# Performance work log

Measured on AMD Instinct MI355X. Metric: run time of the kernel, lower is better.

## Reference

```python
import jax, jax.numpy as jnp
import numpy as np

EPS = 1e-7


def setup_inputs() -> dict:
    key = jax.random.key(0)
    k1, k2, k3 = jax.random.split(key, 3)
    B, Nt, Nv, D = 64, 128, 256, 512
    text_feats = jax.random.normal(k1, (B, Nt, D), dtype=jnp.float32)
    visual_feats = jax.random.normal(k2, (B, Nv, D), dtype=jnp.float32)
    attention_mask = jax.random.randint(k3, (B, Nt), 0, 2, dtype=jnp.int32)
    return {"text_feats": text_feats, "visual_feats": visual_feats,
            "attention_mask": attention_mask}


def _l2norm(x):
    return x / jnp.clip(jnp.linalg.norm(x, axis=-1, keepdims=True), 1e-12)


def reference(text_feats, visual_feats, attention_mask):
    # Normalize token features (F.normalize along D)
    t = _l2norm(text_feats)            # (B, Nt, D)
    v = _l2norm(visual_feats)          # (B, Nv, D)
    # All-pairs token similarities: (B, B, Nt, Nv)
    token_sims = jnp.einsum('itd,jvd->ijtv', t, v)
    # Max over visual tokens -> (B, B, Nt)
    max_sims = jnp.max(token_sims, axis=3)
    # Masked mean over text tokens -> (B, B)
    mask = attention_mask.astype(jnp.float32)[:, None, :]   # (B, 1, Nt) broadcasts over pairs
    masked_sum = jnp.sum(max_sims * mask, axis=2)            # (B, B)
    valid = jnp.clip(jnp.sum(mask, axis=2), EPS)             # (B, 1)
    clip_sims = masked_sum / valid                           # (B, B)
    # Symmetric InfoNCE on the diagonal
    B = clip_sims.shape[0]
    diag = jnp.arange(B)
    losses_t2v = -jax.nn.log_softmax(clip_sims, axis=1)[diag, diag]
    losses_v2t = -jax.nn.log_softmax(clip_sims.T, axis=1)[diag, diag]
    contrastive_loss = jnp.mean(losses_t2v + losses_v2t) / 2.0
    # Regularization: keep negative token sims near zero
    neg_sims = jnp.clip(token_sims, -20.0, 0.0)
    reg_loss = 0.15 * jnp.mean(neg_sims ** 2)
    return contrastive_loss + reg_loss
```

## Files before the change

kernel.cpp:

```cpp
#include <hip/hip_runtime.h>
#include <hip/hip_bf16.h>

#define BB 64
#define NT 128
#define NV 256
#define DD 512
#define BK 32
#define EPSF 1e-7f

typedef __attribute__((ext_vector_type(8))) short bf16x8;
typedef __attribute__((ext_vector_type(4))) float f32x4;

__device__ __forceinline__ void glds16(const ushort* g, ushort* l) {
    __builtin_amdgcn_global_load_lds(
        (const __attribute__((address_space(1))) unsigned int*)g,
        (__attribute__((address_space(3))) unsigned int*)l, 16, 0, 0);
}

__global__ __launch_bounds__(256) void k_normalize(
    const float* __restrict__ tf, const float* __restrict__ vf,
    __hip_bfloat16* __restrict__ tn, __hip_bfloat16* __restrict__ vn) {
    int row = blockIdx.x;
    const float* src;
    __hip_bfloat16* dst;
    if (row < BB * NT) {
        src = tf + (size_t)row * DD;
        dst = tn + (size_t)row * DD;
    } else {
        int r = row - BB * NT;
        src = vf + (size_t)r * DD;
        dst = vn + (size_t)r * DD;
    }
    int tid = threadIdx.x;
    float2 x = ((const float2*)src)[tid];
    float ss = x.x * x.x + x.y * x.y;
    #pragma unroll
    for (int off = 32; off; off >>= 1) ss += __shfl_down(ss, off, 64);
    __shared__ float wsum[4];
    int lane = tid & 63, wid = tid >> 6;
    if (lane == 0) wsum[wid] = ss;
    __syncthreads();
    float tot = wsum[0] + wsum[1] + wsum[2] + wsum[3];
    float scale = 1.0f / fmaxf(sqrtf(tot), 1e-12f);
    __hip_bfloat162 o;
    o.x = __float2bfloat16(x.x * scale);
    o.y = __float2bfloat16(x.y * scale);
    ((__hip_bfloat162*)dst)[tid] = o;
}

__global__ __launch_bounds__(512, 2) void k_gemm(
    const __hip_bfloat16* __restrict__ tn, const __hip_bfloat16* __restrict__ vn,
    float* __restrict__ max_sims, float* __restrict__ reg_sum) {
    __shared__ ushort sT[NT][BK];
    __shared__ ushort sV[NV][BK];
    __shared__ float maxbuf[NT][4];
    __shared__ float redw[8];

    const int i = blockIdx.x, j = blockIdx.y;
    const int tid = threadIdx.x;
    const int l = tid & 63, w = tid >> 6;
    const int wr = w >> 2, wc = w & 3;
    const int m15 = l & 15, q = l >> 4;

    const ushort* tbase = (const ushort*)tn + (size_t)i * NT * DD;
    const ushort* vbase = (const ushort*)vn + (size_t)j * NV * DD;

    const int tf0 = tid * 8;
    const int tr = tf0 >> 5, tc = tf0 & 31;
    const int vf0a = tid * 8;
    const int vra = vf0a >> 5, vca = vf0a & 31;
    const int vf0b = (512 + tid) * 8;
    const int vrb = vf0b >> 5, vcb = vf0b & 31;

    f32x4 acc[4][4];
    #pragma unroll
    for (int rt = 0; rt < 4; ++rt)
        #pragma unroll
        for (int ct = 0; ct < 4; ++ct) acc[rt][ct] = (f32x4){0.f, 0.f, 0.f, 0.f};

    ushort* sTf = &sT[0][0];
    ushort* sVf = &sV[0][0];

    for (int kk = 0; kk < DD; kk += BK) {
        glds16(tbase + (size_t)tr * DD + kk + tc, sTf + tf0);
        glds16(vbase + (size_t)vra * DD + kk + vca, sVf + vf0a);
        glds16(vbase + (size_t)vrb * DD + kk + vcb, sVf + vf0b);
        __syncthreads();

        bf16x8 a[4], b[4];
        #pragma unroll
        for (int rt = 0; rt < 4; ++rt)
            a[rt] = *(const bf16x8*)&sT[wr * 64 + rt * 16 + m15][q * 8];
        #pragma unroll
        for (int ct = 0; ct < 4; ++ct)
            b[ct] = *(const bf16x8*)&sV[wc * 64 + ct * 16 + m15][q * 8];
        #pragma unroll
        for (int rt = 0; rt < 4; ++rt)
            #pragma unroll
            for (int ct = 0; ct < 4; ++ct)
                acc[rt][ct] = __builtin_amdgcn_mfma_f32_16x16x32_bf16(
                    a[rt], b[ct], acc[rt][ct], 0, 0, 0);
        __syncthreads();
    }

    float rp = 0.0f;
    #pragma unroll
    for (int rt = 0; rt < 4; ++rt)
        #pragma unroll
        for (int ct = 0; ct < 4; ++ct)
            #pragma unroll
            for (int r = 0; r < 4; ++r) {
                float m = fminf(acc[rt][ct][r], 0.0f);
                rp = fmaf(m, m, rp);
            }

    #pragma unroll
    for (int rt = 0; rt < 4; ++rt)
        #pragma unroll
        for (int r = 0; r < 4; ++r) {
            float m = acc[rt][0][r];
            #pragma unroll
            for (int ct = 1; ct < 4; ++ct) m = fmaxf(m, acc[rt][ct][r]);
            #pragma unroll
            for (int msk = 1; msk < 16; msk <<= 1)
                m = fmaxf(m, __shfl_xor(m, msk, 64));
            if (m15 == 0)
                maxbuf[wr * 64 + rt * 16 + q * 4 + r][wc] = m;
        }

    #pragma unroll
    for (int off = 32; off; off >>= 1) rp += __shfl_down(rp, off, 64);
    if (l == 0) redw[w] = rp;
    __syncthreads();

    if (tid < NT) {
        float m = fmaxf(fmaxf(maxbuf[tid][0], maxbuf[tid][1]),
                        fmaxf(maxbuf[tid][2], maxbuf[tid][3]));
        max_sims[((size_t)(i * BB + j)) * NT + tid] = m;
    }
    if (tid == 0) {
        float s = 0.0f;
        #pragma unroll
        for (int x = 0; x < 8; ++x) s += redw[x];
        atomicAdd(reg_sum, s);
    }
}

__global__ __launch_bounds__(NT) void k_clip(
    const float* __restrict__ max_sims, const int* __restrict__ mask,
    float* __restrict__ clip_sims) {
    int bx = blockIdx.x;
    int i = bx / BB;
    int t = threadIdx.x;
    float m = (float)mask[i * NT + t];
    float v = max_sims[(size_t)bx * NT + t] * m;
    #pragma unroll
    for (int off = 32; off; off >>= 1) {
        v += __shfl_down(v, off, 64);
        m += __shfl_down(m, off, 64);
    }
    __shared__ float a0[2], a1[2];
    int wid = t >> 6;
    if ((t & 63) == 0) { a0[wid] = v; a1[wid] = m; }
    __syncthreads();
    if (t == 0)
        clip_sims[bx] = (a0[0] + a0[1]) / fmaxf(a1[0] + a1[1], EPSF);
}

__global__ __launch_bounds__(256) void k_loss(
    const float* __restrict__ clip_sims, const float* __restrict__ reg_sum,
    float* __restrict__ out) {
    __shared__ float sc[BB][BB + 1];
    __shared__ float lrow[BB], lcol[BB];
    int tid = threadIdx.x;
    for (int idx = tid; idx < BB * BB; idx += 256)
        sc[idx / BB][idx % BB] = clip_sims[idx];
    __syncthreads();
    if (tid < BB) {
        int i = tid;
        float m = sc[i][0];
        #pragma unroll
        for (int j = 1; j < BB; ++j) m = fmaxf(m, sc[i][j]);
        float s = 0.0f;
        #pragma unroll
        for (int j = 0; j < BB; ++j) s += expf(sc[i][j] - m);
        lrow[i] = m + logf(s) - sc[i][i];
    } else if (tid < 2 * BB) {
        int i = tid - BB;
        float m = sc[0][i];
        #pragma unroll
        for (int j = 1; j < BB; ++j) m = fmaxf(m, sc[j][i]);
        float s = 0.0f;
        #pragma unroll
        for (int j = 0; j < BB; ++j) s += expf(sc[j][i] - m);
        lcol[i] = m + logf(s) - sc[i][i];
    }
    __syncthreads();
    if (tid == 0) {
        float tot = 0.0f;
        for (int i = 0; i < BB; ++i) tot += lrow[i] + lcol[i];
        float contrastive = tot / (2.0f * BB);
        double denom = (double)BB * BB * NT * NV;
        float reg = 0.15f * (float)((double)reg_sum[0] / denom);
        out[0] = contrastive + reg;
    }
}

extern "C" void kernel_launch(void* const* d_in, const int* in_sizes, int n_in,
                              void* d_out, int out_size, void* d_ws, size_t ws_size,
                              hipStream_t stream) {
    const float* tf = (const float*)d_in[0];
    const float* vf = (const float*)d_in[1];
    const int* mask = (const int*)d_in[2];
    float* out = (float*)d_out;

    char* ws = (char*)d_ws;
    size_t tn_bytes = (size_t)BB * NT * DD * sizeof(__hip_bfloat16);
    size_t vn_bytes = (size_t)BB * NV * DD * sizeof(__hip_bfloat16);
    size_t ms_bytes = (size_t)BB * BB * NT * sizeof(float);
    size_t cs_bytes = (size_t)BB * BB * sizeof(float);

    __hip_bfloat16* tn = (__hip_bfloat16*)ws;
    __hip_bfloat16* vn = (__hip_bfloat16*)(ws + tn_bytes);
    float* max_sims = (float*)(ws + tn_bytes + vn_bytes);
    float* clip_sims = (float*)(ws + tn_bytes + vn_bytes + ms_bytes);
    float* reg_sum = (float*)(ws + tn_bytes + vn_bytes + ms_bytes + cs_bytes);

    hipMemsetAsync(reg_sum, 0, sizeof(float), stream);

    k_normalize<<<BB * NT + BB * NV, 256, 0, stream>>>(tf, vf, tn, vn);
    k_gemm<<<dim3(BB, BB), 512, 0, stream>>>(tn, vn, max_sims, reg_sum);
    k_clip<<<BB * BB, NT, 0, stream>>>(max_sims, mask, clip_sims);
    k_loss<<<1, 256, 0, stream>>>(clip_sims, reg_sum, out);
}
```

Before: 272.9 us.

## Fuse masked mean into GEMM, use 256-thread blocks, and swizzle LDS tiles

After: 258.5 us. -5.3%, faster.

```diff
diff --git a/kernel.cpp b/kernel.cpp
--- a/kernel.cpp
+++ b/kernel.cpp
@@ -19,8 +19,10 @@
 
 __global__ __launch_bounds__(256) void k_normalize(
     const float* __restrict__ tf, const float* __restrict__ vf,
-    __hip_bfloat16* __restrict__ tn, __hip_bfloat16* __restrict__ vn) {
+    __hip_bfloat16* __restrict__ tn, __hip_bfloat16* __restrict__ vn,
+    float* __restrict__ reg_sum) {
     int row = blockIdx.x;
+    if (row == 0 && threadIdx.x == 0) *reg_sum = 0.0f;
     const float* src;
     __hip_bfloat16* dst;
     if (row < BB * NT) {
@@ -48,56 +50,85 @@
     ((__hip_bfloat162*)dst)[tid] = o;
 }
 
-__global__ __launch_bounds__(512, 2) void k_gemm(
+__global__ __launch_bounds__(256, 2) void k_gemm(
     const __hip_bfloat16* __restrict__ tn, const __hip_bfloat16* __restrict__ vn,
-    float* __restrict__ max_sims, float* __restrict__ reg_sum) {
+    const int* __restrict__ mask,
+    float* __restrict__ clip_sims, float* __restrict__ reg_sum) {
     __shared__ ushort sT[NT][BK];
     __shared__ ushort sV[NV][BK];
-    __shared__ float maxbuf[NT][4];
-    __shared__ float redw[8];
+    __shared__ float maxbuf[NT][2];
+    __shared__ float redw[4];
+    __shared__ float c0[2], c1[2];
 
     const int i = blockIdx.x, j = blockIdx.y;
     const int tid = threadIdx.x;
     const int l = tid & 63, w = tid >> 6;
-    const int wr = w >> 2, wc = w & 3;
+    const int wr = w >> 1, wc = w & 1;
     const int m15 = l & 15, q = l >> 4;
 
     const ushort* tbase = (const ushort*)tn + (size_t)i * NT * DD;
     const ushort* vbase = (const ushort*)vn + (size_t)j * NV * DD;
 
-    const int tf0 = tid * 8;
-    const int tr = tf0 >> 5, tc = tf0 & 31;
-    const int vf0a = tid * 8;
-    const int vra = vf0a >> 5, vca = vf0a & 31;
-    const int vf0b = (512 + tid) * 8;
-    const int vrb = vf0b >> 5, vcb = vf0b & 31;
-
-    f32x4 acc[4][4];
-    #pragma unroll
-    for (int rt = 0; rt < 4; ++rt)
-        #pragma unroll
-        for (int ct = 0; ct < 4; ++ct) acc[rt][ct] = (f32x4){0.f, 0.f, 0.f, 0.f};
-
     ushort* sTf = &sT[0][0];
     ushort* sVf = &sV[0][0];
 
+    int t_off[2], t_l[2];
+    #pragma unroll
+    for (int s = 0; s < 2; ++s) {
+        int f = s * 256 + tid;
+        int r = f >> 2, qp = f & 3;
+        int qs = qp ^ ((r >> 1) & 3);
+        t_off[s] = r * DD + qs * 8;
+        t_l[s] = f * 8;
+    }
+    int v_off[4], v_l[4];
+    #pragma unroll
+    for (int s = 0; s < 4; ++s) {
+        int f = s * 256 + tid;
+        int r = f >> 2, qp = f & 3;
+        int qs = qp ^ ((r >> 1) & 3);
+        v_off[s] = r * DD + qs * 8;
+        v_l[s] = f * 8;
+    }
+
+    int a_idx[4], b_idx[8];
+    #pragma unroll
+    for (int rt = 0; rt < 4; ++rt) {
+        int row = wr * 64 + rt * 16 + m15;
+        int qp = q ^ ((row >> 1) & 3);
+        a_idx[rt] = row * BK + qp * 8;
+    }
+    #pragma unroll
+    for (int ct = 0; ct < 8; ++ct) {
+        int row = wc * 128 + ct * 16 + m15;
+        int qp = q ^ ((row >> 1) & 3);
+        b_idx[ct] = row * BK + qp * 8;
+    }
+
+    f32x4 acc[4][8];
+    #pragma unroll
+    for (int rt = 0; rt < 4; ++rt)
+        #pragma unroll
+        for (int ct = 0; ct < 8; ++ct) acc[rt][ct] = (f32x4){0.f, 0.f, 0.f, 0.f};
+
     for (int kk = 0; kk < DD; kk += BK) {
-        glds16(tbase + (size_t)tr * DD + kk + tc, sTf + tf0);
-        glds16(vbase + (size_t)vra * DD + kk + vca, sVf + vf0a);
-        glds16(vbase + (size_t)vrb * DD + kk + vcb, sVf + vf0b);
+        #pragma unroll
+        for (int s = 0; s < 2; ++s)
+            glds16(tbase + t_off[s] + kk, sTf + t_l[s]);
+        #pragma unroll
+        for (int s = 0; s < 4; ++s)
+            glds16(vbase + v_off[s] + kk, sVf + v_l[s]);
         __syncthreads();
 
-        bf16x8 a[4], b[4];
+        bf16x8 a[4], b[8];
+        #pragma unroll
+        for (int rt = 0; rt < 4; ++rt) a[rt] = *(const bf16x8*)(sTf + a_idx[rt]);
+        #pragma unroll
+        for (int ct = 0; ct < 8; ++ct) b[ct] = *(const bf16x8*)(sVf + b_idx[ct]);
         #pragma unroll
         for (int rt = 0; rt < 4; ++rt)
-            a[rt] = *(const bf16x8*)&sT[wr * 64 + rt * 16 + m15][q * 8];
-        #pragma unroll
-        for (int ct = 0; ct < 4; ++ct)
-            b[ct] = *(const bf16x8*)&sV[wc * 64 + ct * 16 + m15][q * 8];
-        #pragma unroll
-        for (int rt = 0; rt < 4; ++rt)
-            #pragma unroll
-            for (int ct = 0; ct < 4; ++ct)
+            #pragma unroll
+            for (int ct = 0; ct < 8; ++ct)
                 acc[rt][ct] = __builtin_amdgcn_mfma_f32_16x16x32_bf16(
                     a[rt], b[ct], acc[rt][ct], 0, 0, 0);
         __syncthreads();
@@ -107,7 +138,7 @@
     #pragma unroll
     for (int rt = 0; rt < 4; ++rt)
         #pragma unroll
-        for (int ct = 0; ct < 4; ++ct)
+        for (int ct = 0; ct < 8; ++ct)
             #pragma unroll
             for (int r = 0; r < 4; ++r) {
                 float m = fminf(acc[rt][ct][r], 0.0f);
@@ -120,7 +151,7 @@
         for (int r = 0; r < 4; ++r) {
             float m = acc[rt][0][r];
             #pragma unroll
-            for (int ct = 1; ct < 4; ++ct) m = fmaxf(m, acc[rt][ct][r]);
+            for (int ct = 1; ct < 8; ++ct) m = fmaxf(m, acc[rt][ct][r]);
             #pragma unroll
             for (int msk = 1; msk < 16; msk <<= 1)
                 m = fmaxf(m, __shfl_xor(m, msk, 64));
@@ -134,37 +165,21 @@
     __syncthreads();
 
     if (tid < NT) {
-        float m = fmaxf(fmaxf(maxbuf[tid][0], maxbuf[tid][1]),
-                        fmaxf(maxbuf[tid][2], maxbuf[tid][3]));
-        max_sims[((size_t)(i * BB + j)) * NT + tid] = m;
-    }
+        float rm = fmaxf(maxbuf[tid][0], maxbuf[tid][1]);
+        float mf = (float)mask[i * NT + tid];
+        float v = rm * mf;
+        #pragma unroll
+        for (int off = 32; off; off >>= 1) {
+            v += __shfl_down(v, off, 64);
+            mf += __shfl_down(mf, off, 64);
+        }
+        if (l == 0) { c0[w] = v; c1[w] = mf; }
+    }
+    __syncthreads();
     if (tid == 0) {
-        float s = 0.0f;
-        #pragma unroll
-        for (int x = 0; x < 8; ++x) s += redw[x];
-        atomicAdd(reg_sum, s);
-    }
-}
-
-__global__ __launch_bounds__(NT) void k_clip(
-    const float* __restrict__ max_sims, const int* __restrict__ mask,
-    float* __restrict__ clip_sims) {
-    int bx = blockIdx.x;
-    int i = bx / BB;
-    int t = threadIdx.x;
-    float m = (float)mask[i * NT + t];
-    float v = max_sims[(size_t)bx * NT + t] * m;
-    #pragma unroll
-    for (int off = 32; off; off >>= 1) {
-        v += __shfl_down(v, off, 64);
-        m += __shfl_down(m, off, 64);
-    }
-    __shared__ float a0[2], a1[2];
-    int wid = t >> 6;
-    if ((t & 63) == 0) { a0[wid] = v; a1[wid] = m; }
-    __syncthreads();
-    if (t == 0)
-        clip_sims[bx] = (a0[0] + a0[1]) / fmaxf(a1[0] + a1[1], EPSF);
+        clip_sims[i * BB + j] = (c0[0] + c0[1]) / fmaxf(c1[0] + c1[1], EPSF);
+        atomicAdd(reg_sum, redw[0] + redw[1] + redw[2] + redw[3]);
+    }
 }
 
 __global__ __launch_bounds__(256) void k_loss(
@@ -217,19 +232,14 @@
     char* ws = (char*)d_ws;
     size_t tn_bytes = (size_t)BB * NT * DD * sizeof(__hip_bfloat16);
     size_t vn_bytes = (size_t)BB * NV * DD * sizeof(__hip_bfloat16);
-    size_t ms_bytes = (size_t)BB * BB * NT * sizeof(float);
     size_t cs_bytes = (size_t)BB * BB * sizeof(float);
 
     __hip_bfloat16* tn = (__hip_bfloat16*)ws;
     __hip_bfloat16* vn = (__hip_bfloat16*)(ws + tn_bytes);
-    float* max_sims = (float*)(ws + tn_bytes + vn_bytes);
-    float* clip_sims = (float*)(ws + tn_bytes + vn_bytes + ms_bytes);
-    float* reg_sum = (float*)(ws + tn_bytes + vn_bytes + ms_bytes + cs_bytes);
-
-    hipMemsetAsync(reg_sum, 0, sizeof(float), stream);
-
-    k_normalize<<<BB * NT + BB * NV, 256, 0, stream>>>(tf, vf, tn, vn);
-    k_gemm<<<dim3(BB, BB), 512, 0, stream>>>(tn, vn, max_sims, reg_sum);
-    k_clip<<<BB * BB, NT, 0, stream>>>(max_sims, mask, clip_sims);
+    float* clip_sims = (float*)(ws + tn_bytes + vn_bytes);
+    float* reg_sum = (float*)(ws + tn_bytes + vn_bytes + cs_bytes);
+
+    k_normalize<<<BB * NT + BB * NV, 256, 0, stream>>>(tf, vf, tn, vn, reg_sum);
+    k_gemm<<<dim3(BB, BB), 256, 0, stream>>>(tn, vn, mask, clip_sims, reg_sum);
     k_loss<<<1, 256, 0, stream>>>(clip_sims, reg_sum, out);
 }
```
